# Kernel optimization log

Measured on AMD Instinct MI355X. Metric: run time of the kernel, lower is better.

The kernel has to match this reference:

```python
import jax, jax.numpy as jnp
import numpy as np

SW = 4096      # sliding_window
NH = 32        # n_heads
NKV = 8        # n_kv_heads
HD = 128       # head_dim
HIDDEN = 4096
B = 32         # batch (= max_batch_size)
GROUP = NH // NKV


def _nearest_32(n):
    return ((n + 31) // 32) * 32


def setup_inputs() -> dict:
    key = jax.random.key(0)
    ks = jax.random.split(key, 6)
    START = 5000  # start_pos > sliding_window -> wrapped-cache mask branch
    x = jax.random.normal(ks[0], (1, 1, B, HIDDEN), jnp.float32)
    wqkv = jax.random.normal(ks[1], (HIDDEN, (NH + 2 * NKV) * HD), jnp.float32) * 0.02
    wo = jax.random.normal(ks[2], (NH * HD, HIDDEN), jnp.float32) * 0.02
    cache_k = jax.random.normal(ks[3], (B, NKV, SW, HD), jnp.float32)
    cache_v = jax.random.normal(ks[4], (B, NKV, SW, HD), jnp.float32)
    # rotation matrix (freqs_to_rotation_matrix equivalent): block rotation for pos=START
    half = HD // 2
    inv_freq = 1.0 / (10000.0 ** (jnp.arange(half, dtype=jnp.float32) * 2.0 / HD))
    ang = START * inv_freq
    cos, sin = jnp.cos(ang), jnp.sin(ang)
    idx = jnp.arange(half)
    R = jnp.zeros((HD, HD), jnp.float32)
    R = R.at[idx, idx].set(cos).at[idx + half, idx + half].set(cos)
    R = R.at[idx, idx + half].set(sin).at[idx + half, idx].set(-sin)
    rot_mat = jnp.tile(R[None, None], (1, B, 1, 1))  # (1, B, HD, HD)
    # attention mask exactly as prepare_inputs builds it
    current = START % SW
    P = min(_nearest_32(START + 1), SW)
    NEG = jnp.finfo(jnp.float32).min
    mask = jnp.zeros((1, NH, B, P), jnp.float32)
    if START < SW:
        mask = mask.at[..., current + 1:].set(NEG)
    else:
        mask = mask.at[..., :current].set(NEG)
        mask = mask.at[..., SW - current:].set(NEG)
    return {"x": x, "rot_mat": rot_mat, "attn_mask": mask,
            "cache_k": cache_k, "cache_v": cache_v,
            "wqkv": wqkv, "wo": wo, "start_pos": START}


def reference(x, rot_mat, attn_mask, cache_k, cache_v, wqkv, wo, start_pos):
    P = min(_nearest_32(start_pos + 1), SW)    # padded_layer_past_len
    current = start_pos % SW                   # write slot in the ring cache
    # fused QKV projection: (1,1,B,H) @ (H,6144) -> take the (B,6144) slice
    xqkv = jnp.einsum('stbh,hf->stbf', x, wqkv)[0, 0]
    q = xqkv[:, :NH * HD].reshape(B, NH, HD)
    k = xqkv[:, NH * HD:(NH + NKV) * HD].reshape(B, NKV, HD)
    v = xqkv[:, (NH + NKV) * HD:].reshape(B, NKV, HD)
    # rotary via per-batch rotation matrix bmm
    R = rot_mat[0]                              # (B, HD, HD)
    q = jnp.einsum('bhd,bde->bhe', q, R)
    k = jnp.einsum('bkd,bde->bke', k, R)
    # update ring KV cache at slot `current`
    cache_k = cache_k.at[:, :, current, :].set(k)
    cache_v = cache_v.at[:, :, current, :].set(v)
    keys = cache_k[:, :, :P, :]                 # (B, NKV, P, HD)
    values = cache_v[:, :, :P, :]
    # grouped-query attention: q heads grouped per kv head
    qg = q.reshape(B, NKV, GROUP, HD)
    scores = jnp.einsum('bkgd,bkpd->bkgp', qg, keys) * (1.0 / np.sqrt(HD))
    # attn_mask is (1, NH, B, P); reorder to (B, NKV, GROUP, P)
    mask = jnp.transpose(attn_mask[0].reshape(NKV, GROUP, B, P), (2, 0, 1, 3))
    probs = jax.nn.softmax(scores + mask, axis=-1)
    out = jnp.einsum('bkgp,bkpd->bkgd', probs, values).reshape(B, NH * HD)
    dense = out @ wo                            # (B, HIDDEN)
    return dense.reshape(1, 1, B, HIDDEN)
```

## Files before the change

### kernel.cpp

```cpp
#include <hip/hip_runtime.h>
#include <hip/hip_bf16.h>
#include <stdint.h>

#define SW 4096
#define NH 32
#define NKV 8
#define GROUP 4
#define HD 128
#define HIDDEN 4096
#define BB 32
#define NQKV ((NH + 2*NKV)*HD)
#define CH 512
#define CHP (CH + 4)
#define NCH 8

template<int NW>
__global__ __launch_bounds__(256)
void gemm_f32(const float* __restrict__ A, const float* __restrict__ W,
              float* __restrict__ part, int kchunk) {
    const int n0 = blockIdx.x * 256;
    const int K0 = blockIdx.y * kchunk;
    const int t = threadIdx.x;
    const int tm = t >> 6;
    const int tn = t & 63;
    __shared__ float a_lds[32*36];
    __shared__ float w_lds[32*256];

    float acc[8][4];
    #pragma unroll
    for (int i = 0; i < 8; ++i)
        #pragma unroll
        for (int j = 0; j < 4; ++j) acc[i][j] = 0.f;

    for (int ks = 0; ks < kchunk; ks += 32) {
        {
            int m = t & 31, kl = t >> 5;
            #pragma unroll
            for (int i = 0; i < 4; ++i) {
                int k = kl + i*8;
                a_lds[k*36 + m] = A[(size_t)m*HIDDEN + K0 + ks + k];
            }
        }
        {
            #pragma unroll
            for (int i = 0; i < 8; ++i) {
                int j = t + i*256;
                int k = j >> 6, c = j & 63;
                const float4* src = (const float4*)(W + (size_t)(K0 + ks + k)*NW + n0);
                *(float4*)&w_lds[k*256 + c*4] = src[c];
            }
        }
        __syncthreads();
        #pragma unroll 8
        for (int k = 0; k < 32; ++k) {
            float4 a0 = *(const float4*)&a_lds[k*36 + tm*8];
            float4 a1 = *(const float4*)&a_lds[k*36 + tm*8 + 4];
            float4 w  = *(const float4*)&w_lds[k*256 + tn*4];
            float am[8] = {a0.x,a0.y,a0.z,a0.w,a1.x,a1.y,a1.z,a1.w};
            #pragma unroll
            for (int mi = 0; mi < 8; ++mi) {
                acc[mi][0] += am[mi]*w.x;
                acc[mi][1] += am[mi]*w.y;
                acc[mi][2] += am[mi]*w.z;
                acc[mi][3] += am[mi]*w.w;
            }
        }
        __syncthreads();
    }
    float* dst = part + (size_t)blockIdx.y*32*NW;
    #pragma unroll
    for (int mi = 0; mi < 8; ++mi) {
        int m = tm*8 + mi;
        float4 v = make_float4(acc[mi][0], acc[mi][1], acc[mi][2], acc[mi][3]);
        *(float4*)&dst[(size_t)m*NW + n0 + tn*4] = v;
    }
}

template<int NW>
__global__ __launch_bounds__(256)
void reduce_part(const float* __restrict__ part, float* __restrict__ out, int ksplit) {
    int idx = blockIdx.x*256 + threadIdx.x;
    if (idx >= 32*NW) return;
    float s = 0.f;
    for (int i = 0; i < ksplit; ++i) s += part[(size_t)i*32*NW + idx];
    out[idx] = s;
}

__global__ __launch_bounds__(256)
void rope_red(const float* __restrict__ part1, int KS, const float* __restrict__ rot,
              float* __restrict__ qrot, float* __restrict__ krot) {
    const int b = blockIdx.x;
    const int hbase = blockIdx.y * 8;
    const int t = threadIdx.x;
    __shared__ float Rl[64 * HD];
    __shared__ float qin[8 * HD];
    {
        const float* qsrc = part1 + (size_t)b * NQKV + (size_t)hbase * HD;
        float4 a = make_float4(0.f, 0.f, 0.f, 0.f);
        for (int i = 0; i < KS; ++i) {
            float4 v = ((const float4*)(qsrc + (size_t)i * 32 * NQKV))[t];
            a.x += v.x; a.y += v.y; a.z += v.z; a.w += v.w;
        }
        ((float4*)qin)[t] = a;
    }

    float acc[4] = {0.f, 0.f, 0.f, 0.f};
    for (int pass = 0; pass < 2; ++pass) {
        const float4* rsrc = (const float4*)(rot + (size_t)b * HD * HD + pass * 64 * HD);
        #pragma unroll
        for (int i = 0; i < 8; ++i) {
            int j = t + i * 256;
            ((float4*)Rl)[j] = rsrc[j];
        }
        __syncthreads();
        #pragma unroll
        for (int i = 0; i < 4; ++i) {
            int o = t + i * 256;
            int h = o >> 7, e = o & 127;
            float s = 0.f;
            for (int d = 0; d < 64; ++d) s += qin[h * HD + pass * 64 + d] * Rl[d * HD + e];
            acc[i] += s;
        }
        __syncthreads();
    }
    #pragma unroll
    for (int i = 0; i < 4; ++i) {
        int o = t + i * 256;
        int h = o >> 7, e = o & 127;
        int hh = hbase + h;
        if (hh < NH) qrot[((size_t)b * NH + hh) * HD + e] = acc[i];
        else         krot[((size_t)b * NKV + (hh - NH)) * HD + e] = acc[i];
    }
}

__device__ __forceinline__ void window_of(int sp, int& lo, int& hi, int& cur) {
    cur = ((sp % SW) + SW) % SW;
    if (sp < SW) { lo = 0; hi = sp + 1; } else { lo = cur; hi = SW - cur; }
}

__global__ __launch_bounds__(256)
void attn_chunk(const float* __restrict__ qrot, const float* __restrict__ krot,
                const float* __restrict__ part1, int KS,
                const float* __restrict__ ck, const float* __restrict__ cv,
                const int* __restrict__ spp, float* __restrict__ attnp) {
    const int bkv = blockIdx.x;
    const int b = bkv >> 3, kv = bkv & 7;
    const int c = blockIdx.y;
    const int t = threadIdx.x;
    int lo, hi, cur;
    window_of(spp[0], lo, hi, cur);
    const int n = hi - lo;
    const int base0 = c * CH;
    if (base0 >= n) return;
    const int nc = (n - base0 < CH) ? (n - base0) : CH;
    const size_t kvoff = (size_t)(b * NKV + kv) * SW * HD;
    const float scale = 0.08838834764831845f;

    __shared__ float q_lds[GROUP * HD];
    __shared__ float scl[GROUP * CHP];
    __shared__ float vnew[HD];
    __shared__ float mg[GROUP], lg[GROUP];
    __shared__ float pp[4][GROUP][HD];

    {
        const size_t qoff = ((size_t)b * NH + kv * GROUP) * HD;
        q_lds[t]       = qrot[qoff + t];
        q_lds[256 + t] = qrot[qoff + 256 + t];
    }
    if (t < HD) {
        const float* vsrc = part1 + (size_t)b * NQKV + (size_t)(NH + NKV) * HD + kv * HD + t;
        float s = 0.f;
        for (int i = 0; i < KS; ++i) s += vsrc[(size_t)i * 32 * NQKV];
        vnew[t] = s;
    }
    __syncthreads();

    {
        const int dsl  = t & 7;
        const int posw = (t >> 3) & 7;
        const int w    = t >> 6;
        float4 qreg[GROUP][4];
        #pragma unroll
        for (int g = 0; g < GROUP; ++g)
            #pragma unroll
            for (int j = 0; j < 4; ++j)
                qreg[g][j] = *(const float4*)&q_lds[g*HD + j*32 + dsl*4];

        const float* krow = krot + ((size_t)b * NKV + kv) * HD;
        #pragma unroll 1
        for (int it = 0; it < CH/32; ++it) {
            const int r = it*32 + w*8 + posw;
            const bool valid = (r < nc);
            float s0 = 0.f, s1 = 0.f, s2 = 0.f, s3 = 0.f;
            if (valid) {
                const int p = lo + base0 + r;
                const float* kbase = (p == cur) ? krow : (ck + kvoff + (size_t)p * HD);
                #pragma unroll
                for (int j = 0; j < 4; ++j) {
                    float4 kk = *(const float4*)&kbase[j*32 + dsl*4];
                    s0 += kk.x*qreg[0][j].x + kk.y*qreg[0][j].y + kk.z*qreg[0][j].z + kk.w*qreg[0][j].w;
                    s1 += kk.x*qreg[1][j].x + kk.y*qreg[1][j].y + kk.z*qreg[1][j].z + kk.w*qreg[1][j].w;
                    s2 += kk.x*qreg[2][j].x + kk.y*qreg[2][j].y + kk.z*qreg[2][j].z + kk.w*qreg[2][j].w;
                    s3 += kk.x*qreg[3][j].x + kk.y*qreg[3][j].y + kk.z*qreg[3][j].z + kk.w*qreg[3][j].w;
                }
            }
            s0 += __shfl_xor(s0, 1); s0 += __shfl_xor(s0, 2); s0 += __shfl_xor(s0, 4);
            s1 += __shfl_xor(s1, 1); s1 += __shfl_xor(s1, 2); s1 += __shfl_xor(s1, 4);
            s2 += __shfl_xor(s2, 1); s2 += __shfl_xor(s2, 2); s2 += __shfl_xor(s2, 4);
            s3 += __shfl_xor(s3, 1); s3 += __shfl_xor(s3, 2); s3 += __shfl_xor(s3, 4);
            float sg = (dsl == 0) ? s0 : (dsl == 1) ? s1 : (dsl == 2) ? s2 : s3;
            if (dsl < GROUP)
                scl[dsl * CHP + r] = valid ? sg * scale : -3.0e38f;
        }
    }
    __syncthreads();

    {
        const int w = t >> 6, l = t & 63;
        float v[8];
        float m = -3.0e38f;
        #pragma unroll
        for (int j = 0; j < 8; ++j) {
            v[j] = scl[w*CHP + l + 64*j];
            m = fmaxf(m, v[j]);
        }
        #pragma unroll
        for (int off = 32; off; off >>= 1) m = fmaxf(m, __shfl_xor(m, off));
        float ss = 0.f;
        #pragma unroll
        for (int j = 0; j < 8; ++j) {
            float e = __expf(v[j] - m);
            scl[w*CHP + l + 64*j] = e;
            ss += e;
        }
        #pragma unroll
        for (int off = 32; off; off >>= 1) ss += __shfl_xor(ss, off);
        if (l == 0) { mg[w] = m; lg[w] = ss; }
    }
    __syncthreads();

    {
        const int d2 = (t & 63) * 2, rg = t >> 6;
        const int r0 = rg * (CH/4);
        const float2 vn2 = *(const float2*)&vnew[d2];
        float a0[GROUP], a1[GROUP];
        #pragma unroll
        for (int g = 0; g < GROUP; ++g) { a0[g] = 0.f; a1[g] = 0.f; }
        #pragma unroll 1
        for (int i = 0; i < CH/16; ++i) {
            const int r = r0 + i*4;
            float4 pr[GROUP];
            #pragma unroll
            for (int g = 0; g < GROUP; ++g)
                pr[g] = *(const float4*)&scl[g*CHP + r];
            #pragma unroll
            for (int k = 0; k < 4; ++k) {
                const int rr = r + k;
                const int p = lo + base0 + rr;
                float2 v;
                if (rr >= nc)      v = make_float2(0.f, 0.f);
                else if (p == cur) v = vn2;
                else               v = *(const float2*)&cv[kvoff + (size_t)p * HD + d2];
                const float p0 = (k == 0) ? pr[0].x : (k == 1) ? pr[0].y : (k == 2) ? pr[0].z : pr[0].w;
                const float p1 = (k == 0) ? pr[1].x : (k == 1) ? pr[1].y : (k == 2) ? pr[1].z : pr[1].w;
                const float p2 = (k == 0) ? pr[2].x : (k == 1) ? pr[2].y : (k == 2) ? pr[2].z : pr[2].w;
                const float p3 = (k == 0) ? pr[3].x : (k == 1) ? pr[3].y : (k == 2) ? pr[3].z : pr[3].w;
                a0[0] += p0 * v.x; a1[0] += p0 * v.y;
                a0[1] += p1 * v.x; a1[1] += p1 * v.y;
                a0[2] += p2 * v.x; a1[2] += p2 * v.y;
                a0[3] += p3 * v.x; a1[3] += p3 * v.y;
            }
        }
        #pragma unroll
        for (int g = 0; g < GROUP; ++g) {
            pp[rg][g][d2]     = a0[g];
            pp[rg][g][d2 + 1] = a1[g];
        }
    }
    __syncthreads();
    {
        float* op = attnp + ((size_t)bkv * NCH + c) * 520;
        #pragma unroll
        for (int j = 0; j < 2; ++j) {
            int v = t + 256*j;
            int g = v >> 7, d = v & 127;
            op[g * HD + d] = pp[0][g][d] + pp[1][g][d] + pp[2][g][d] + pp[3][g][d];
        }
        if (t < GROUP) {
            op[512 + t] = mg[t];
            op[516 + t] = lg[t];
        }
    }
}

__global__ __launch_bounds__(512)
void attn_reduce(const float* __restrict__ attnp, const int* __restrict__ spp,
                 float* __restrict__ aout) {
    const int bkv = blockIdx.x;
    const int b = bkv >> 3, kv = bkv & 7;
    const int g = threadIdx.x >> 7, d = threadIdx.x & 127;
    int lo, hi, cur;
    window_of(spp[0], lo, hi, cur);
    const int n = hi - lo;
    const int nch = (n + CH - 1) / CH;
    float M = -3.0e38f;
    for (int c = 0; c < nch; ++c)
        M = fmaxf(M, attnp[((size_t)bkv * NCH + c) * 520 + 512 + g]);
    float L = 0.f, O = 0.f;
    for (int c = 0; c < nch; ++c) {
        const float* op = attnp + ((size_t)bkv * NCH + c) * 520;
        float w = __expf(op[512 + g] - M);
        L += w * op[516 + g];
        O += w * op[g * HD + d];
    }
    aout[(size_t)b * NH * HD + (size_t)(kv * GROUP + g) * HD + d] = O / L;
}

__global__ __launch_bounds__(512)
void attn_kernel(const float* __restrict__ qrot, const float* __restrict__ krot,
                 const float* __restrict__ qkv,
                 const float* __restrict__ ck, const float* __restrict__ cv,
                 const int* __restrict__ spp, float* __restrict__ aout) {
    const int b = blockIdx.x >> 3, kv = blockIdx.x & 7;
    const int t = threadIdx.x;
    int lo, hi, cur;
    window_of(spp[0], lo, hi, cur);
    const int n = hi - lo;
    const size_t kvoff = (size_t)(b * NKV + kv) * SW * HD;
    const float scale = 0.08838834764831845f;

    __shared__ float sc[GROUP * 2304];
    __shared__ float q_lds[GROUP * HD];
    __shared__ float redb[512];
    __shared__ float ssum_s[GROUP];

    q_lds[t] = qrot[((size_t)b * NH + kv * GROUP) * HD + t];
    __syncthreads();

    for (int i = t; i < n; i += 512) {
        int p = lo + i;
        float s[GROUP] = {0.f, 0.f, 0.f, 0.f};
        if (p == cur) {
            const float* kr = krot + ((size_t)b * NKV + kv) * HD;
            for (int d = 0; d < HD; ++d) {
                float kd = kr[d];
                #pragma unroll
                for (int g = 0; g < GROUP; ++g) s[g] += kd * q_lds[g * HD + d];
            }
        } else {
            const float* kp = ck + kvoff + (size_t)p * HD;
            for (int c = 0; c < 32; ++c) {
                float4 kk = ((const float4*)kp)[c];
                #pragma unroll
                for (int g = 0; g < GROUP; ++g)
                    s[g] += kk.x * q_lds[g * HD + c * 4] + kk.y * q_lds[g * HD + c * 4 + 1]
                          + kk.z * q_lds[g * HD + c * 4 + 2] + kk.w * q_lds[g * HD + c * 4 + 3];
            }
        }
        #pragma unroll
        for (int g = 0; g < GROUP; ++g)
            sc[g * 2304 + i] = s[g] * scale;
    }
    __syncthreads();

    for (int g = 0; g < GROUP; ++g) {
        float m = -3.0e38f;
        for (int i = t; i < n; i += 512) m = fmaxf(m, sc[g * 2304 + i]);
        redb[t] = m;
        __syncthreads();
        for (int w = 256; w > 0; w >>= 1) {
            if (t < w) redb[t] = fmaxf(redb[t], redb[t + w]);
            __syncthreads();
        }
        float mx = redb[0];
        __syncthreads();
        float s = 0.f;
        for (int i = t; i < n; i += 512) {
            float e = __expf(sc[g * 2304 + i] - mx);
            sc[g * 2304 + i] = e;
            s += e;
        }
        redb[t] = s;
        __syncthreads();
        for (int w = 256; w > 0; w >>= 1) {
            if (t < w) redb[t] += redb[t + w];
            __syncthreads();
        }
        if (t == 0) ssum_s[g] = redb[0];
        __syncthreads();
    }

    {
        const int g = t >> 7, d = t & 127;
        const float vn = qkv[(size_t)b * NQKV + (size_t)(NH + NKV) * HD + kv * HD + d];
        float acc = 0.f;
        for (int r = 0; r < n; ++r) {
            int p = lo + r;
            float v = (p == cur) ? vn : cv[kvoff + (size_t)p * HD + d];
            acc += sc[g * 2304 + r] * v;
        }
        aout[(size_t)b * NH * HD + (size_t)(kv * GROUP + g) * HD + d] = acc / ssum_s[g];
    }
}

extern "C" void kernel_launch(void* const* d_in, const int* in_sizes, int n_in,
                              void* d_out, int out_size, void* d_ws, size_t ws_size,
                              hipStream_t stream) {
    (void)out_size;
    static const long long CS[8] = {131072LL, 524288LL, 4194304LL, 134217728LL,
                                    134217728LL, 25165824LL, 16777216LL, 1LL};
    const void* Pp[8];
    bool canonical = (n_in == 8);
    if (canonical)
        for (int i = 0; i < 8; ++i)
            if ((long long)in_sizes[i] != CS[i]) { canonical = false; break; }
    if (canonical) {
        for (int i = 0; i < 8; ++i) Pp[i] = d_in[i];
    } else {
        bool used[64] = {false};
        for (int j = 0; j < 8; ++j) {
            Pp[j] = d_in[0];
            for (int i = 0; i < n_in && i < 64; ++i)
                if (!used[i] && (long long)in_sizes[i] == CS[j]) { used[i] = true; Pp[j] = d_in[i]; break; }
        }
    }

    const float* x    = (const float*)Pp[0];
    const float* rot  = (const float*)Pp[1];
    const float* ck   = (const float*)Pp[3];
    const float* cv   = (const float*)Pp[4];
    const float* wqkv = (const float*)Pp[5];
    const float* wo   = (const float*)Pp[6];
    const int*   sp   = (const int*)Pp[7];

    float* qkv  = (float*)d_ws;
    float* qrot = qkv  + (size_t)BB*NQKV;
    float* krot = qrot + (size_t)BB*NH*HD;
    float* aout = krot + (size_t)BB*NKV*HD;
    float* attnp= aout + (size_t)BB*NH*HD;
    float* part1= attnp + (size_t)BB*NKV*NCH*520;

    const size_t head_bytes = ((size_t)BB*(NQKV + NH*HD + NKV*HD + NH*HD)
                               + (size_t)BB*NKV*NCH*520) * 4;
    const size_t p1_bytes   = (size_t)16*32*NQKV*4;
    const size_t p2_bytes   = (size_t)32*32*HIDDEN*4;

    if (ws_size >= head_bytes + p1_bytes + p2_bytes) {
        const int KS1 = 16, KS2 = 32;
        float* part2 = part1 + (size_t)KS1*32*NQKV;

        gemm_f32<NQKV><<<dim3(NQKV/256, KS1), 256, 0, stream>>>(x, wqkv, part1, HIDDEN/KS1);
        rope_red<<<dim3(BB, 5), 256, 0, stream>>>(part1, KS1, rot, qrot, krot);
        attn_chunk<<<dim3(BB*NKV, NCH), 256, 0, stream>>>(qrot, krot, part1, KS1, ck, cv, sp, attnp);
        attn_reduce<<<BB*NKV, 512, 0, stream>>>(attnp, sp, aout);
        gemm_f32<HIDDEN><<<dim3(HIDDEN/256, KS2), 256, 0, stream>>>(aout, wo, part2, HIDDEN/KS2);
        reduce_part<HIDDEN><<<(BB*HIDDEN + 255)/256, 256, 0, stream>>>(part2, (float*)d_out, KS2);
    } else {
        size_t per_ks = (size_t)32*(NQKV + HIDDEN) * 4;
        size_t avail = (ws_size > head_bytes) ? ws_size - head_bytes : 0;
        int KS = 1;
        if      (avail >= 8*per_ks) KS = 8;
        else if (avail >= 4*per_ks) KS = 4;
        else if (avail >= 2*per_ks) KS = 2;
        float* part2 = part1 + (size_t)KS*32*NQKV;

        gemm_f32<NQKV><<<dim3(NQKV/256, KS), 256, 0, stream>>>(x, wqkv, part1, HIDDEN/KS);
        reduce_part<NQKV><<<(BB*NQKV + 255)/256, 256, 0, stream>>>(part1, qkv, KS);
        rope_red<<<dim3(BB, 5), 256, 0, stream>>>(part1, KS, rot, qrot, krot);
        attn_kernel<<<BB*NKV, 512, 0, stream>>>(qrot, krot, qkv, ck, cv, sp, aout);
        gemm_f32<HIDDEN><<<dim3(HIDDEN/256, KS), 256, 0, stream>>>(aout, wo, part2, HIDDEN/KS);
        reduce_part<HIDDEN><<<(BB*HIDDEN + 255)/256, 256, 0, stream>>>(part2, (float*)d_out, KS);
    }
}
```

Measured before the change: 237.9 us.

## Use direct global-to-LDS loads in GEMM, trim attention loops, raise QKV split-K

```diff
diff --git a/kernel.cpp b/kernel.cpp
--- a/kernel.cpp
+++ b/kernel.cpp
@@ -14,6 +14,15 @@
 #define CHP (CH + 4)
 #define NCH 8
 
+#if defined(__has_builtin)
+#if __has_builtin(__builtin_amdgcn_global_load_lds)
+#define HAS_GLL 1
+#endif
+#endif
+#ifndef HAS_GLL
+#define HAS_GLL 0
+#endif
+
 template<int NW>
 __global__ __launch_bounds__(256)
 void gemm_f32(const float* __restrict__ A, const float* __restrict__ W,
@@ -41,6 +50,19 @@
                 a_lds[k*36 + m] = A[(size_t)m*HIDDEN + K0 + ks + k];
             }
         }
+#if HAS_GLL
+        {
+            #pragma unroll
+            for (int i = 0; i < 8; ++i) {
+                int j = t + i*256;
+                int k = j >> 6, c = j & 63;
+                __builtin_amdgcn_global_load_lds(
+                    (const __attribute__((address_space(1))) void*)(W + (size_t)(K0 + ks + k)*NW + n0 + (c<<2)),
+                    (__attribute__((address_space(3))) void*)(&w_lds[k*256 + (c<<2)]),
+                    16, 0, 0);
+            }
+        }
+#else
         {
             #pragma unroll
             for (int i = 0; i < 8; ++i) {
@@ -50,6 +72,7 @@
                 *(float4*)&w_lds[k*256 + c*4] = src[c];
             }
         }
+#endif
         __syncthreads();
         #pragma unroll 8
         for (int k = 0; k < 32; ++k) {
@@ -175,6 +198,8 @@
     }
     __syncthreads();
 
+    const int iters = (nc + 31) >> 5;
+
     {
         const int dsl  = t & 7;
         const int posw = (t >> 3) & 7;
@@ -188,7 +213,7 @@
 
         const float* krow = krot + ((size_t)b * NKV + kv) * HD;
         #pragma unroll 1
-        for (int it = 0; it < CH/32; ++it) {
+        for (int it = 0; it < iters; ++it) {
             const int r = it*32 + w*8 + posw;
             const bool valid = (r < nc);
             float s0 = 0.f, s1 = 0.f, s2 = 0.f, s3 = 0.f;
@@ -212,6 +237,9 @@
             if (dsl < GROUP)
                 scl[dsl * CHP + r] = valid ? sg * scale : -3.0e38f;
         }
+        for (int r = (iters << 5) + t; r < CH; r += 256)
+            #pragma unroll
+            for (int g = 0; g < GROUP; ++g) scl[g*CHP + r] = -3.0e38f;
     }
     __syncthreads();
 
@@ -242,12 +270,14 @@
     {
         const int d2 = (t & 63) * 2, rg = t >> 6;
         const int r0 = rg * (CH/4);
+        const int nrows = (nc > r0) ? ((nc - r0 < CH/4) ? nc - r0 : CH/4) : 0;
+        const int imax = (nrows + 3) >> 2;
         const float2 vn2 = *(const float2*)&vnew[d2];
         float a0[GROUP], a1[GROUP];
         #pragma unroll
         for (int g = 0; g < GROUP; ++g) { a0[g] = 0.f; a1[g] = 0.f; }
         #pragma unroll 1
-        for (int i = 0; i < CH/16; ++i) {
+        for (int i = 0; i < imax; ++i) {
             const int r = r0 + i*4;
             float4 pr[GROUP];
             #pragma unroll
@@ -442,11 +472,11 @@
 
     const size_t head_bytes = ((size_t)BB*(NQKV + NH*HD + NKV*HD + NH*HD)
                                + (size_t)BB*NKV*NCH*520) * 4;
-    const size_t p1_bytes   = (size_t)16*32*NQKV*4;
+    const size_t p1_bytes   = (size_t)32*32*NQKV*4;
     const size_t p2_bytes   = (size_t)32*32*HIDDEN*4;
 
     if (ws_size >= head_bytes + p1_bytes + p2_bytes) {
-        const int KS1 = 16, KS2 = 32;
+        const int KS1 = 32, KS2 = 32;
         float* part2 = part1 + (size_t)KS1*32*NQKV;
 
         gemm_f32<NQKV><<<dim3(NQKV/256, KS1), 256, 0, stream>>>(x, wqkv, part1, HIDDEN/KS1);
```

After: 308.6 us. 29.7% more time.
